# Kernel tuning notes

Measured on AMD Instinct MI355X. Metric: run time of the kernel, lower is better.

The kernel has to match this reference:

```python
import jax, jax.numpy as jnp
import numpy as np

N, B, F_IN, T = 500, 8, 8, 12      # nodes, batch, in_feats, time_interval
H1 = H2 = H3 = 16                   # GCN layer widths (must be equal; see source bug)
HID = 8                             # per-node GRU hidden
E = 8000                            # edges
HG = N * HID                        # GRU hidden size  = 4000
IG = N * H3                         # GRU input size   = 8000


def setup_inputs() -> dict:
    key = jax.random.key(0)
    ks = jax.random.split(key, 12)
    inputs = jax.random.normal(ks[0], (N, B, F_IN, T), jnp.float32)
    src = jax.random.randint(ks[1], (E,), 0, N)
    dst = jax.random.randint(ks[2], (E,), 0, N)

    def lin(k, fi, fo):
        return jax.random.normal(k, (fi, fo), jnp.float32) / np.float32(np.sqrt(fi))

    W1 = lin(ks[3], F_IN, H1); b1 = jax.random.normal(ks[4], (H1,), jnp.float32) * 0.01
    W2 = lin(ks[5], H1, H2);   b2 = jax.random.normal(ks[6], (H2,), jnp.float32) * 0.01
    W3 = lin(ks[7], H2, H3);   b3 = jax.random.normal(ks[8], (H3,), jnp.float32) * 0.01
    W_ih = jax.random.normal(ks[9], (3 * HG, IG), jnp.float32) / np.float32(np.sqrt(IG))
    W_hh = jax.random.normal(ks[10], (3 * HG, HG), jnp.float32) / np.float32(np.sqrt(HG))
    b_ih = jax.random.normal(ks[11], (3 * HG,), jnp.float32) * 0.01
    b_hh = jnp.zeros((3 * HG,), jnp.float32)
    return {"inputs": inputs, "src": src, "dst": dst,
            "W1": W1, "b1": b1, "W2": W2, "b2": b2, "W3": W3, "b3": b3,
            "W_ih": W_ih, "W_hh": W_hh, "b_ih": b_ih, "b_hh": b_hh}


def reference(inputs, src, dst, W1, b1, W2, b2, W3, b3, W_ih, W_hh, b_ih, b_hh):
    ones_e = jnp.ones((E,), jnp.float32)
    # DGL GraphConv norm='both': D_out^{-1/2} on source, D_in^{-1/2} on dest, degs clamped >= 1
    n_out = jnp.clip(jax.ops.segment_sum(ones_e, src, num_segments=N), 1.0) ** -0.5
    n_in = jnp.clip(jax.ops.segment_sum(ones_e, dst, num_segments=N), 1.0) ** -0.5

    def gconv(x, W, b):  # x: [N, B, F]
        m = x * n_out[:, None, None]
        agg = jax.ops.segment_sum(m[src], dst, num_segments=N)
        return (agg * n_in[:, None, None]) @ W + b

    def gcn(x):  # one timestep [N, B, F_IN] -> [N, B, H3]
        h = jax.nn.relu(gconv(x, W1, b1))
        h = jax.nn.relu(gconv(h, W2, b2))
        return gconv(h, W3, b3)

    g = jax.vmap(gcn)(jnp.moveaxis(inputs, 3, 0))        # [T, N, B, H3]
    x_seq = jnp.transpose(g, (0, 2, 1, 3)).reshape(T, B, IG)  # [T, B, N*H3]

    def step(h, x):  # PyTorch GRU cell, gate order r, z, n
        gi = x @ W_ih.T + b_ih
        gh = h @ W_hh.T + b_hh
        i_r, i_z, i_n = jnp.split(gi, 3, axis=-1)
        h_r, h_z, h_n = jnp.split(gh, 3, axis=-1)
        r = jax.nn.sigmoid(i_r + h_r)
        z = jax.nn.sigmoid(i_z + h_z)
        n = jnp.tanh(i_n + r * h_n)
        return (1.0 - z) * n + z * h, None

    h0 = jnp.zeros((B, HG), inputs.dtype)
    hT, _ = jax.lax.scan(step, h0, x_seq)
    return hT.reshape(B, N, HID)
```

## Files before the change

### kernel.cpp

```cpp
#include <hip/hip_runtime.h>

#define NN 500
#define BB 8
#define FIN 8
#define TT 12
#define HH 16
#define EE 8000
#define HG 4000
#define IG 8000
#define G3 12000
#define MM 96

typedef __attribute__((ext_vector_type(8))) _Float16 half8;
typedef __attribute__((ext_vector_type(4))) _Float16 half4v;
typedef __attribute__((ext_vector_type(4))) float f32x4;

__global__ __launch_bounds__(512) void k_prep(const int* __restrict__ src,
                                              const int* __restrict__ dst,
                                              float* __restrict__ n_out,
                                              float* __restrict__ n_in,
                                              int* __restrict__ row_ptr,
                                              int* __restrict__ edge_src) {
  __shared__ int s_dout[NN];
  __shared__ int s_din[NN];
  __shared__ int s_off[NN + 1];
  int tid = threadIdx.x;
  for (int i = tid; i < NN; i += 512) { s_dout[i] = 0; s_din[i] = 0; }
  __syncthreads();
  for (int e = tid; e < EE; e += 512) {
    atomicAdd(&s_dout[src[e]], 1);
    atomicAdd(&s_din[dst[e]], 1);
  }
  __syncthreads();
  if (tid == 0) {
    int acc = 0;
    for (int n = 0; n < NN; ++n) { s_off[n] = acc; acc += s_din[n]; }
    s_off[NN] = acc;
  }
  __syncthreads();
  for (int i = tid; i < NN; i += 512) {
    int dv = s_dout[i]; if (dv < 1) dv = 1;
    int iv = s_din[i];  if (iv < 1) iv = 1;
    n_out[i] = rsqrtf((float)dv);
    n_in[i]  = rsqrtf((float)iv);
    row_ptr[i] = s_off[i];
  }
  if (tid == 0) row_ptr[NN] = s_off[NN];
  __syncthreads();
  for (int e = tid; e < EE; e += 512) {
    int d = dst[e];
    int pos = atomicAdd(&s_off[d], 1);
    edge_src[pos] = src[e];
  }
}

__global__ __launch_bounds__(256) void k_transpose(const float* __restrict__ in,
                                                   float* __restrict__ out) {
  int idx = blockIdx.x * 256 + threadIdx.x;
  if (idx >= TT * NN * BB * FIN) return;
  int f = idx % FIN;
  int b = (idx / FIN) % BB;
  int n = (idx / (FIN * BB)) % NN;
  int t = idx / (FIN * BB * NN);
  out[idx] = in[((n * BB + b) * FIN + f) * TT + t];
}

template <int FI, int FO, bool RELU, typename OT, bool OUT_SEQ>
__global__ __launch_bounds__(128) void k_gcn(const float* __restrict__ x,
                                             const float* __restrict__ W,
                                             const float* __restrict__ bias,
                                             const float* __restrict__ n_out,
                                             const float* __restrict__ n_in,
                                             const int* __restrict__ row_ptr,
                                             const int* __restrict__ edge_src,
                                             OT* __restrict__ y) {
  int bid = blockIdx.x;
  int t = bid / NN, n = bid % NN;
  __shared__ float sW[FI * FO];
  __shared__ float sB[FO];
  __shared__ float sAgg[BB * FI];
  int tid = threadIdx.x;
  for (int i = tid; i < FI * FO; i += 128) sW[i] = W[i];
  if (tid < FO) sB[tid] = bias[tid];
  int r0 = row_ptr[n], r1 = row_ptr[n + 1];
  if (tid < BB * FI) {
    int b = tid / FI, fi = tid % FI;
    float acc = 0.f;
    for (int p = r0; p < r1; ++p) {
      int s = edge_src[p];
      acc += x[((t * NN + s) * BB + b) * FI + fi] * n_out[s];
    }
    sAgg[tid] = acc * n_in[n];
  }
  __syncthreads();
  if (tid < BB * FO) {
    int b = tid / FO, fo = tid % FO;
    float v = sB[fo];
#pragma unroll
    for (int fi = 0; fi < FI; ++fi) v += sAgg[b * FI + fi] * sW[fi * FO + fo];
    if (RELU) v = fmaxf(v, 0.f);
    int oidx = OUT_SEQ ? (((t * BB + b) * NN + n) * FO + fo)
                       : (((t * NN + n) * BB + b) * FO + fo);
    y[oidx] = (OT)v;
  }
}

__global__ __launch_bounds__(256) void k_cvt_whh(const float* __restrict__ w,
                                                 _Float16* __restrict__ wh) {
  size_t i8 = ((size_t)blockIdx.x * 256 + threadIdx.x) * 8;
  if (i8 >= (size_t)G3 * HG) return;
  float4 a = *(const float4*)(w + i8);
  float4 b = *(const float4*)(w + i8 + 4);
  half8 h;
  h[0] = (_Float16)a.x; h[1] = (_Float16)a.y; h[2] = (_Float16)a.z; h[3] = (_Float16)a.w;
  h[4] = (_Float16)b.x; h[5] = (_Float16)b.y; h[6] = (_Float16)b.z; h[7] = (_Float16)b.w;
  *(half8*)(wh + i8) = h;
}

__global__ __launch_bounds__(256, 3) void k_gemm_gi_mfma(const _Float16* __restrict__ Xh,
                                                         const float* __restrict__ Wih,
                                                         float* __restrict__ gip) {
  __shared__ _Float16 sXh[96 * 40];
  __shared__ _Float16 sWh[32 * 40];
  int tid = threadIdx.x;
  int wave = tid >> 6, lane = tid & 63;
  int jb = blockIdx.x * 32;
  int kbase = blockIdx.y * 4000;

  int xrow[3], xc4[3];
  const ushort4* px[3];
#pragma unroll
  for (int i = 0; i < 3; ++i) {
    int idx = i * 256 + tid;
    xrow[i] = idx >> 3; xc4[i] = idx & 7;
    px[i] = (const ushort4*)(Xh + (size_t)xrow[i] * IG + kbase + xc4[i] * 4);
  }
  int wrow = tid >> 3, wc4 = tid & 7;
  const float4* pw = (const float4*)(Wih + (size_t)(jb + wrow) * IG + kbase + wc4 * 4);

  int jt = wave & 1;
  int mh = wave >> 1;
  f32x4 acc[3] = {{0.f,0.f,0.f,0.f},{0.f,0.f,0.f,0.f},{0.f,0.f,0.f,0.f}};

  ushort4 xr[3]; float4 wr;
#pragma unroll
  for (int i = 0; i < 3; ++i) xr[i] = px[i][0];
  wr = pw[0];

  int l15 = lane & 15;
  int colh = (lane >> 4) * 8;

  for (int c = 0; c < 125; ++c) {
    __syncthreads();
#pragma unroll
    for (int i = 0; i < 3; ++i)
      *(ushort4*)&sXh[xrow[i] * 40 + xc4[i] * 4] = xr[i];
    {
      half4v h;
      h[0] = (_Float16)wr.x; h[1] = (_Float16)wr.y;
      h[2] = (_Float16)wr.z; h[3] = (_Float16)wr.w;
      *(half4v*)&sWh[wrow * 40 + wc4 * 4] = h;
    }
    __syncthreads();
    if (c < 124) {
#pragma unroll
      for (int i = 0; i < 3; ++i) xr[i] = px[i][(c + 1) * 8];
      wr = pw[(c + 1) * 8];
    }
    half8 bfrag = *(const half8*)&sWh[(jt * 16 + l15) * 40 + colh];
#pragma unroll
    for (int t = 0; t < 3; ++t) {
      half8 afrag = *(const half8*)&sXh[(mh * 48 + t * 16 + l15) * 40 + colh];
      acc[t] = __builtin_amdgcn_mfma_f32_16x16x32_f16(afrag, bfrag, acc[t], 0, 0, 0);
    }
  }

  float* out = gip + (size_t)blockIdx.y * (MM * G3);
  int j = jb + jt * 16 + l15;
#pragma unroll
  for (int t = 0; t < 3; ++t) {
    int mb = mh * 48 + t * 16 + (lane >> 4) * 4;
#pragma unroll
    for (int r = 0; r < 4; ++r)
      out[(size_t)(mb + r) * G3 + j] = acc[t][r];
  }
}

__device__ __forceinline__ int swz2(int f) { return f ^ (((f >> 4) & 7) << 1); }

__global__ __launch_bounds__(256) void k_gemm_gh(const float* __restrict__ ht,
                                                 const _Float16* __restrict__ Whh_h,
                                                 float* __restrict__ ghp) {
  int j0 = blockIdx.x * 96;
  int ks = blockIdx.y;
  int kbase = ks * 1000;
  __shared__ float4 sH4[2000];
  int tid = threadIdx.x;
  const float4* H4 = (const float4*)ht;
#pragma unroll
  for (int l = 0; l < 8; ++l) {
    int f = l * 256 + tid;
    if (f < 2000) sH4[swz2(f)] = H4[kbase * 2 + f];
  }
  __syncthreads();
  int jl = tid >> 3;
  int k8 = tid & 7;
  const half8* W0 = (const half8*)(Whh_h + (size_t)(j0 + jl)      * HG + kbase);
  const half8* W1 = (const half8*)(Whh_h + (size_t)(j0 + jl + 32) * HG + kbase);
  const half8* W2 = (const half8*)(Whh_h + (size_t)(j0 + jl + 64) * HG + kbase);
  float acc[3][8] = {};
  for (int i = 0; i < 16; ++i) {
    int kq = i * 8 + k8;
    if (kq < 125) {
      half8 w0 = W0[kq], w1 = W1[kq], w2 = W2[kq];
#pragma unroll
      for (int kk = 0; kk < 8; ++kk) {
        int f = (kq * 8 + kk) * 2;
        float4 ha = sH4[swz2(f)];
        float4 hb = sH4[swz2(f + 1)];
        float hm[8] = {ha.x, ha.y, ha.z, ha.w, hb.x, hb.y, hb.z, hb.w};
        float v0 = (float)w0[kk], v1 = (float)w1[kk], v2 = (float)w2[kk];
#pragma unroll
        for (int m = 0; m < 8; ++m) {
          acc[0][m] += hm[m] * v0;
          acc[1][m] += hm[m] * v1;
          acc[2][m] += hm[m] * v2;
        }
      }
    }
  }
#pragma unroll
  for (int r = 0; r < 3; ++r)
#pragma unroll
    for (int m = 0; m < 8; ++m) {
      float v = acc[r][m];
      v += __shfl_down(v, 4, 8);
      v += __shfl_down(v, 2, 8);
      v += __shfl_down(v, 1, 8);
      acc[r][m] = v;
    }
  if (k8 == 0) {
    float* outp = ghp + (size_t)ks * (BB * G3);
#pragma unroll
    for (int r = 0; r < 3; ++r) {
      int j = j0 + jl + r * 32;
#pragma unroll
      for (int m = 0; m < 8; ++m) outp[m * G3 + j] = acc[r][m];
    }
  }
}

__global__ __launch_bounds__(256) void k_gates0(const float* __restrict__ gip,
                                                const float* __restrict__ b_ih,
                                                const float* __restrict__ b_hh,
                                                float* __restrict__ h32n) {
  int idx = blockIdx.x * 256 + threadIdx.x;
  int q = idx >> 3, m = idx & 7;
  const float* g0 = gip + (size_t)m * G3;
  const float* g1 = gip + (size_t)MM * G3 + (size_t)m * G3;
  float ir  = b_ih[q]          + g0[q]          + g1[q];
  float iz  = b_ih[q + HG]     + g0[q + HG]     + g1[q + HG];
  float in_ = b_ih[q + 2*HG]   + g0[q + 2*HG]   + g1[q + 2*HG];
  float r = 1.f / (1.f + __expf(-(ir + b_hh[q])));
  float z = 1.f / (1.f + __expf(-(iz + b_hh[q + HG])));
  float nn = tanhf(in_ + r * b_hh[q + 2*HG]);
  h32n[idx] = (1.f - z) * nn;
}

__global__ __launch_bounds__(256) void k_gates(const float* __restrict__ gip,
                                               const float* __restrict__ ghp,
                                               const float* __restrict__ b_ih,
                                               const float* __restrict__ b_hh,
                                               const float* __restrict__ ht_old,
                                               float* __restrict__ ht_new,
                                               float* __restrict__ hout, int t) {
  int idx = blockIdx.x * 256 + threadIdx.x;
  if (idx >= BB * HG) return;
  int b = idx / HG, q = idx % HG;
  int m = t * BB + b;
  const float* g0 = gip;
  const float* g1 = gip + (size_t)MM * G3;
  float ir = b_ih[q]          + g0[m * G3 + q]          + g1[m * G3 + q];
  float iz = b_ih[q + HG]     + g0[m * G3 + q + HG]     + g1[m * G3 + q + HG];
  float in_ = b_ih[q + 2*HG]  + g0[m * G3 + q + 2*HG]   + g1[m * G3 + q + 2*HG];
  float hr = b_hh[q], hz = b_hh[q + HG], hn = b_hh[q + 2*HG];
#pragma unroll
  for (int s = 0; s < 4; ++s) {
    const float* gh = ghp + (size_t)s * (BB * G3) + b * G3;
    hr += gh[q]; hz += gh[q + HG]; hn += gh[q + 2*HG];
  }
  float r = 1.f / (1.f + __expf(-(ir + hr)));
  float z = 1.f / (1.f + __expf(-(iz + hz)));
  float nn = tanhf(in_ + r * hn);
  float ho = ht_old[q * BB + b];
  float h = (1.f - z) * nn + z * ho;
  ht_new[q * BB + b] = h;
  if (hout) hout[b * HG + q] = h;
}

extern "C" void kernel_launch(void* const* d_in, const int* in_sizes, int n_in,
                              void* d_out, int out_size, void* d_ws, size_t ws_size,
                              hipStream_t stream) {
  const float* x_in = (const float*)d_in[0];
  const int*   src  = (const int*)d_in[1];
  const int*   dst  = (const int*)d_in[2];
  const float* W1   = (const float*)d_in[3];
  const float* b1   = (const float*)d_in[4];
  const float* W2   = (const float*)d_in[5];
  const float* b2   = (const float*)d_in[6];
  const float* W3   = (const float*)d_in[7];
  const float* b3   = (const float*)d_in[8];
  const float* Wih  = (const float*)d_in[9];
  const float* Whh  = (const float*)d_in[10];
  const float* bih  = (const float*)d_in[11];
  const float* bhh  = (const float*)d_in[12];
  float* out = (float*)d_out;

  float* W = (float*)d_ws;
  size_t off = 0;
  float* n_out = W + off; off += 512;
  float* n_in_ = W + off; off += 512;
  float* x0    = W + off; off += (size_t)TT * NN * BB * FIN;
  float* xa    = W + off; off += (size_t)TT * NN * BB * HH;
  float* xb    = W + off; off += (size_t)TT * NN * BB * HH;
  _Float16* xseq = (_Float16*)(W + off); off += (size_t)MM * IG / 2;
  float* gip   = W + off; off += (size_t)2 * MM * G3;
  float* ghp   = W + off; off += (size_t)4 * BB * G3;
  float* ht0   = W + off; off += (size_t)HG * BB;
  float* ht1   = W + off; off += (size_t)HG * BB;
  int* row_ptr  = (int*)(W + off); off += 512;
  int* edge_src = (int*)(W + off); off += 8000;
  off = (off + 3) & ~(size_t)3;
  _Float16* whh_h = (_Float16*)(W + off); off += (size_t)G3 * HG / 2;
  (void)ws_size; (void)in_sizes; (void)n_in; (void)out_size;

  k_cvt_whh<<<((size_t)G3 * HG / 8 + 255) / 256, 256, 0, stream>>>(Whh, whh_h);
  k_prep<<<1, 512, 0, stream>>>(src, dst, n_out, n_in_, row_ptr, edge_src);
  k_transpose<<<(TT * NN * BB * FIN + 255) / 256, 256, 0, stream>>>(x_in, x0);
  k_gcn<FIN, HH, true, float, false><<<TT * NN, 128, 0, stream>>>(x0, W1, b1, n_out, n_in_, row_ptr, edge_src, xa);
  k_gcn<HH, HH, true, float, false><<<TT * NN, 128, 0, stream>>>(xa, W2, b2, n_out, n_in_, row_ptr, edge_src, xb);
  k_gcn<HH, HH, false, _Float16, true><<<TT * NN, 128, 0, stream>>>(xb, W3, b3, n_out, n_in_, row_ptr, edge_src, xseq);
  k_gemm_gi_mfma<<<dim3(375, 2), 256, 0, stream>>>(xseq, Wih, gip);

  k_gates0<<<BB * HG / 256, 256, 0, stream>>>(gip, bih, bhh, ht0);

  float* hcur = ht0;
  float* hnxt = ht1;
  for (int t = 1; t < TT; ++t) {
    k_gemm_gh<<<dim3(125, 4), 256, 0, stream>>>(hcur, whh_h, ghp);
    k_gates<<<(BB * HG + 255) / 256, 256, 0, stream>>>(
        gip, ghp, bih, bhh, hcur, hnxt, (t == TT - 1) ? out : nullptr, t);
    float* tmp = hcur; hcur = hnxt; hnxt = tmp;
  }
}
```

Before: 525.9 us.

## Fuse recurrent GEMM and GRU gate update via last-block split-K reduction

Merges the per-timestep hidden-state GEMM and the gate kernel into one kernel. Each block now computes all three gates (r, z, n) for the same 32 hidden units, so the last of the four split-K blocks can reduce the partials and apply the gates in place, using an atomic counter per column group. This removes 11 kernel launches and the separate gate pass's global round trip. In exchange it adds atomics, fences and a counter reset, and the weight row accesses become strided across the three gate blocks.

```diff
diff --git a/kernel.cpp b/kernel.cpp
--- a/kernel.cpp
+++ b/kernel.cpp
@@ -186,70 +186,6 @@
   }
 }
 
-__device__ __forceinline__ int swz2(int f) { return f ^ (((f >> 4) & 7) << 1); }
-
-__global__ __launch_bounds__(256) void k_gemm_gh(const float* __restrict__ ht,
-                                                 const _Float16* __restrict__ Whh_h,
-                                                 float* __restrict__ ghp) {
-  int j0 = blockIdx.x * 96;
-  int ks = blockIdx.y;
-  int kbase = ks * 1000;
-  __shared__ float4 sH4[2000];
-  int tid = threadIdx.x;
-  const float4* H4 = (const float4*)ht;
-#pragma unroll
-  for (int l = 0; l < 8; ++l) {
-    int f = l * 256 + tid;
-    if (f < 2000) sH4[swz2(f)] = H4[kbase * 2 + f];
-  }
-  __syncthreads();
-  int jl = tid >> 3;
-  int k8 = tid & 7;
-  const half8* W0 = (const half8*)(Whh_h + (size_t)(j0 + jl)      * HG + kbase);
-  const half8* W1 = (const half8*)(Whh_h + (size_t)(j0 + jl + 32) * HG + kbase);
-  const half8* W2 = (const half8*)(Whh_h + (size_t)(j0 + jl + 64) * HG + kbase);
-  float acc[3][8] = {};
-  for (int i = 0; i < 16; ++i) {
-    int kq = i * 8 + k8;
-    if (kq < 125) {
-      half8 w0 = W0[kq], w1 = W1[kq], w2 = W2[kq];
-#pragma unroll
-      for (int kk = 0; kk < 8; ++kk) {
-        int f = (kq * 8 + kk) * 2;
-        float4 ha = sH4[swz2(f)];
-        float4 hb = sH4[swz2(f + 1)];
-        float hm[8] = {ha.x, ha.y, ha.z, ha.w, hb.x, hb.y, hb.z, hb.w};
-        float v0 = (float)w0[kk], v1 = (float)w1[kk], v2 = (float)w2[kk];
-#pragma unroll
-        for (int m = 0; m < 8; ++m) {
-          acc[0][m] += hm[m] * v0;
-          acc[1][m] += hm[m] * v1;
-          acc[2][m] += hm[m] * v2;
-        }
-      }
-    }
-  }
-#pragma unroll
-  for (int r = 0; r < 3; ++r)
-#pragma unroll
-    for (int m = 0; m < 8; ++m) {
-      float v = acc[r][m];
-      v += __shfl_down(v, 4, 8);
-      v += __shfl_down(v, 2, 8);
-      v += __shfl_down(v, 1, 8);
-      acc[r][m] = v;
-    }
-  if (k8 == 0) {
-    float* outp = ghp + (size_t)ks * (BB * G3);
-#pragma unroll
-    for (int r = 0; r < 3; ++r) {
-      int j = j0 + jl + r * 32;
-#pragma unroll
-      for (int m = 0; m < 8; ++m) outp[m * G3 + j] = acc[r][m];
-    }
-  }
-}
-
 __global__ __launch_bounds__(256) void k_gates0(const float* __restrict__ gip,
                                                 const float* __restrict__ b_ih,
                                                 const float* __restrict__ b_hh,
@@ -267,35 +203,113 @@
   h32n[idx] = (1.f - z) * nn;
 }
 
-__global__ __launch_bounds__(256) void k_gates(const float* __restrict__ gip,
-                                               const float* __restrict__ ghp,
-                                               const float* __restrict__ b_ih,
-                                               const float* __restrict__ b_hh,
-                                               const float* __restrict__ ht_old,
-                                               float* __restrict__ ht_new,
-                                               float* __restrict__ hout, int t) {
-  int idx = blockIdx.x * 256 + threadIdx.x;
-  if (idx >= BB * HG) return;
-  int b = idx / HG, q = idx % HG;
-  int m = t * BB + b;
-  const float* g0 = gip;
-  const float* g1 = gip + (size_t)MM * G3;
-  float ir = b_ih[q]          + g0[m * G3 + q]          + g1[m * G3 + q];
-  float iz = b_ih[q + HG]     + g0[m * G3 + q + HG]     + g1[m * G3 + q + HG];
-  float in_ = b_ih[q + 2*HG]  + g0[m * G3 + q + 2*HG]   + g1[m * G3 + q + 2*HG];
-  float hr = b_hh[q], hz = b_hh[q + HG], hn = b_hh[q + 2*HG];
-#pragma unroll
-  for (int s = 0; s < 4; ++s) {
-    const float* gh = ghp + (size_t)s * (BB * G3) + b * G3;
-    hr += gh[q]; hz += gh[q + HG]; hn += gh[q + 2*HG];
-  }
-  float r = 1.f / (1.f + __expf(-(ir + hr)));
-  float z = 1.f / (1.f + __expf(-(iz + hz)));
-  float nn = tanhf(in_ + r * hn);
-  float ho = ht_old[q * BB + b];
-  float h = (1.f - z) * nn + z * ho;
-  ht_new[q * BB + b] = h;
-  if (hout) hout[b * HG + q] = h;
+__device__ __forceinline__ int swz2(int f) { return f ^ (((f >> 4) & 7) << 1); }
+
+__global__ __launch_bounds__(256) void k_ghg(const float* __restrict__ ht,
+                                             const _Float16* __restrict__ Whh_h,
+                                             const float* __restrict__ gip,
+                                             const float* __restrict__ b_ih,
+                                             const float* __restrict__ b_hh,
+                                             float* __restrict__ preS,
+                                             int* __restrict__ cnt,
+                                             float* __restrict__ ht_new,
+                                             float* __restrict__ hout, int t) {
+  int qg = blockIdx.x;
+  int ks = blockIdx.y;
+  int kbase = ks * 1000;
+  __shared__ float4 sH4[2000];
+  __shared__ int sLast;
+  int tid = threadIdx.x;
+  const float4* H4 = (const float4*)ht;
+#pragma unroll
+  for (int l = 0; l < 8; ++l) {
+    int f = l * 256 + tid;
+    if (f < 2000) sH4[swz2(f)] = H4[kbase * 2 + f];
+  }
+  __syncthreads();
+  int jl = tid >> 3;
+  int k8 = tid & 7;
+  int q = qg * 32 + jl;
+  const half8* W0 = (const half8*)(Whh_h + (size_t)q            * HG + kbase);
+  const half8* W1 = (const half8*)(Whh_h + (size_t)(q + HG)     * HG + kbase);
+  const half8* W2 = (const half8*)(Whh_h + (size_t)(q + 2 * HG) * HG + kbase);
+  float acc[3][8] = {};
+  for (int i = 0; i < 16; ++i) {
+    int kq = i * 8 + k8;
+    if (kq < 125) {
+      half8 w0 = W0[kq], w1 = W1[kq], w2 = W2[kq];
+#pragma unroll
+      for (int kk = 0; kk < 8; ++kk) {
+        int f = (kq * 8 + kk) * 2;
+        float4 ha = sH4[swz2(f)];
+        float4 hb = sH4[swz2(f + 1)];
+        float hm[8] = {ha.x, ha.y, ha.z, ha.w, hb.x, hb.y, hb.z, hb.w};
+        float v0 = (float)w0[kk], v1 = (float)w1[kk], v2 = (float)w2[kk];
+#pragma unroll
+        for (int m = 0; m < 8; ++m) {
+          acc[0][m] += hm[m] * v0;
+          acc[1][m] += hm[m] * v1;
+          acc[2][m] += hm[m] * v2;
+        }
+      }
+    }
+  }
+#pragma unroll
+  for (int r = 0; r < 3; ++r)
+#pragma unroll
+    for (int m = 0; m < 8; ++m) {
+      float v = acc[r][m];
+      v += __shfl_down(v, 4, 8);
+      v += __shfl_down(v, 2, 8);
+      v += __shfl_down(v, 1, 8);
+      acc[r][m] = v;
+    }
+  if (k8 == 0) {
+    float* slot = preS + (((size_t)ks * HG + q) * 3) * 8;
+#pragma unroll
+    for (int g = 0; g < 3; ++g)
+#pragma unroll
+      for (int m = 0; m < 8; ++m)
+        __hip_atomic_store(&slot[g * 8 + m], acc[g][m],
+                           __ATOMIC_RELAXED, __HIP_MEMORY_SCOPE_AGENT);
+  }
+  __threadfence();
+  __syncthreads();
+  if (tid == 0) {
+    int old = __hip_atomic_fetch_add(&cnt[qg], 1, __ATOMIC_ACQ_REL,
+                                     __HIP_MEMORY_SCOPE_AGENT);
+    sLast = (old == 3) ? 1 : 0;
+  }
+  __syncthreads();
+  if (!sLast) return;
+  __threadfence();
+  {
+    int ql = tid >> 3, m = tid & 7;
+    int qq = qg * 32 + ql;
+    float hr = b_hh[qq], hz = b_hh[qq + HG], hn = b_hh[qq + 2 * HG];
+#pragma unroll
+    for (int s = 0; s < 4; ++s) {
+      const float* sl = preS + (((size_t)s * HG + qq) * 3) * 8;
+      hr += __hip_atomic_load(&sl[0 * 8 + m], __ATOMIC_RELAXED, __HIP_MEMORY_SCOPE_AGENT);
+      hz += __hip_atomic_load(&sl[1 * 8 + m], __ATOMIC_RELAXED, __HIP_MEMORY_SCOPE_AGENT);
+      hn += __hip_atomic_load(&sl[2 * 8 + m], __ATOMIC_RELAXED, __HIP_MEMORY_SCOPE_AGENT);
+    }
+    int mg = t * BB + m;
+    const float* g0 = gip + (size_t)mg * G3;
+    const float* g1 = gip + (size_t)MM * G3 + (size_t)mg * G3;
+    float ir  = b_ih[qq]          + g0[qq]          + g1[qq];
+    float iz  = b_ih[qq + HG]     + g0[qq + HG]     + g1[qq + HG];
+    float in_ = b_ih[qq + 2*HG]   + g0[qq + 2*HG]   + g1[qq + 2*HG];
+    float r = 1.f / (1.f + __expf(-(ir + hr)));
+    float z = 1.f / (1.f + __expf(-(iz + hz)));
+    float nn = tanhf(in_ + r * hn);
+    float ho = ht[qq * BB + m];
+    float h = (1.f - z) * nn + z * ho;
+    ht_new[qq * BB + m] = h;
+    if (hout) hout[m * HG + qq] = h;
+  }
+  if (tid == 0)
+    __hip_atomic_store(&cnt[qg], 0, __ATOMIC_RELAXED, __HIP_MEMORY_SCOPE_AGENT);
 }
 
 extern "C" void kernel_launch(void* const* d_in, const int* in_sizes, int n_in,
@@ -325,15 +339,17 @@
   float* xb    = W + off; off += (size_t)TT * NN * BB * HH;
   _Float16* xseq = (_Float16*)(W + off); off += (size_t)MM * IG / 2;
   float* gip   = W + off; off += (size_t)2 * MM * G3;
-  float* ghp   = W + off; off += (size_t)4 * BB * G3;
+  float* preS  = W + off; off += (size_t)4 * HG * 3 * 8;
   float* ht0   = W + off; off += (size_t)HG * BB;
   float* ht1   = W + off; off += (size_t)HG * BB;
   int* row_ptr  = (int*)(W + off); off += 512;
   int* edge_src = (int*)(W + off); off += 8000;
+  int* cnt      = (int*)(W + off); off += 128;
   off = (off + 3) & ~(size_t)3;
   _Float16* whh_h = (_Float16*)(W + off); off += (size_t)G3 * HG / 2;
   (void)ws_size; (void)in_sizes; (void)n_in; (void)out_size;
 
+  hipMemsetAsync(cnt, 0, 128 * sizeof(int), stream);
   k_cvt_whh<<<((size_t)G3 * HG / 8 + 255) / 256, 256, 0, stream>>>(Whh, whh_h);
   k_prep<<<1, 512, 0, stream>>>(src, dst, n_out, n_in_, row_ptr, edge_src);
   k_transpose<<<(TT * NN * BB * FIN + 255) / 256, 256, 0, stream>>>(x_in, x0);
@@ -347,9 +363,9 @@
   float* hcur = ht0;
   float* hnxt = ht1;
   for (int t = 1; t < TT; ++t) {
-    k_gemm_gh<<<dim3(125, 4), 256, 0, stream>>>(hcur, whh_h, ghp);
-    k_gates<<<(BB * HG + 255) / 256, 256, 0, stream>>>(
-        gip, ghp, bih, bhh, hcur, hnxt, (t == TT - 1) ? out : nullptr, t);
+    k_ghg<<<dim3(125, 4), 256, 0, stream>>>(hcur, whh_h, gip, bih, bhh,
+                                            preS, cnt, hnxt,
+                                            (t == TT - 1) ? out : nullptr, t);
     float* tmp = hcur; hcur = hnxt; hnxt = tmp;
   }
 }
```

New measurement: 1.243 ms. 136% more time.

## Use MFMA for recurrent W_hh GEMM and fuse weight conversion into first step

Applied to the files above, without the earlier changes.

Replaces the scalar-FMA hidden-state GEMM with an MFMA 16x16x32 f16 kernel. The hidden state is now also written as an fp16 [B,HG] copy by the gate kernels to feed it. The separate W_hh fp32->fp16 conversion kernel is removed; the first recurrent step converts and stores the fp16 weights while it computes, saving one full pass over the weights. This cuts ALU work and launches. In exchange the hidden state enters the GEMM in fp16, and half of each MFMA B tile is wasted on padding rows for the batch of 8.

```diff
diff --git a/kernel.cpp b/kernel.cpp
--- a/kernel.cpp
+++ b/kernel.cpp
@@ -105,18 +105,6 @@
   }
 }
 
-__global__ __launch_bounds__(256) void k_cvt_whh(const float* __restrict__ w,
-                                                 _Float16* __restrict__ wh) {
-  size_t i8 = ((size_t)blockIdx.x * 256 + threadIdx.x) * 8;
-  if (i8 >= (size_t)G3 * HG) return;
-  float4 a = *(const float4*)(w + i8);
-  float4 b = *(const float4*)(w + i8 + 4);
-  half8 h;
-  h[0] = (_Float16)a.x; h[1] = (_Float16)a.y; h[2] = (_Float16)a.z; h[3] = (_Float16)a.w;
-  h[4] = (_Float16)b.x; h[5] = (_Float16)b.y; h[6] = (_Float16)b.z; h[7] = (_Float16)b.w;
-  *(half8*)(wh + i8) = h;
-}
-
 __global__ __launch_bounds__(256, 3) void k_gemm_gi_mfma(const _Float16* __restrict__ Xh,
                                                          const float* __restrict__ Wih,
                                                          float* __restrict__ gip) {
@@ -186,74 +174,11 @@
   }
 }
 
-__device__ __forceinline__ int swz2(int f) { return f ^ (((f >> 4) & 7) << 1); }
-
-__global__ __launch_bounds__(256) void k_gemm_gh(const float* __restrict__ ht,
-                                                 const _Float16* __restrict__ Whh_h,
-                                                 float* __restrict__ ghp) {
-  int j0 = blockIdx.x * 96;
-  int ks = blockIdx.y;
-  int kbase = ks * 1000;
-  __shared__ float4 sH4[2000];
-  int tid = threadIdx.x;
-  const float4* H4 = (const float4*)ht;
-#pragma unroll
-  for (int l = 0; l < 8; ++l) {
-    int f = l * 256 + tid;
-    if (f < 2000) sH4[swz2(f)] = H4[kbase * 2 + f];
-  }
-  __syncthreads();
-  int jl = tid >> 3;
-  int k8 = tid & 7;
-  const half8* W0 = (const half8*)(Whh_h + (size_t)(j0 + jl)      * HG + kbase);
-  const half8* W1 = (const half8*)(Whh_h + (size_t)(j0 + jl + 32) * HG + kbase);
-  const half8* W2 = (const half8*)(Whh_h + (size_t)(j0 + jl + 64) * HG + kbase);
-  float acc[3][8] = {};
-  for (int i = 0; i < 16; ++i) {
-    int kq = i * 8 + k8;
-    if (kq < 125) {
-      half8 w0 = W0[kq], w1 = W1[kq], w2 = W2[kq];
-#pragma unroll
-      for (int kk = 0; kk < 8; ++kk) {
-        int f = (kq * 8 + kk) * 2;
-        float4 ha = sH4[swz2(f)];
-        float4 hb = sH4[swz2(f + 1)];
-        float hm[8] = {ha.x, ha.y, ha.z, ha.w, hb.x, hb.y, hb.z, hb.w};
-        float v0 = (float)w0[kk], v1 = (float)w1[kk], v2 = (float)w2[kk];
-#pragma unroll
-        for (int m = 0; m < 8; ++m) {
-          acc[0][m] += hm[m] * v0;
-          acc[1][m] += hm[m] * v1;
-          acc[2][m] += hm[m] * v2;
-        }
-      }
-    }
-  }
-#pragma unroll
-  for (int r = 0; r < 3; ++r)
-#pragma unroll
-    for (int m = 0; m < 8; ++m) {
-      float v = acc[r][m];
-      v += __shfl_down(v, 4, 8);
-      v += __shfl_down(v, 2, 8);
-      v += __shfl_down(v, 1, 8);
-      acc[r][m] = v;
-    }
-  if (k8 == 0) {
-    float* outp = ghp + (size_t)ks * (BB * G3);
-#pragma unroll
-    for (int r = 0; r < 3; ++r) {
-      int j = j0 + jl + r * 32;
-#pragma unroll
-      for (int m = 0; m < 8; ++m) outp[m * G3 + j] = acc[r][m];
-    }
-  }
-}
-
 __global__ __launch_bounds__(256) void k_gates0(const float* __restrict__ gip,
                                                 const float* __restrict__ b_ih,
                                                 const float* __restrict__ b_hh,
-                                                float* __restrict__ h32n) {
+                                                float* __restrict__ h32n,
+                                                _Float16* __restrict__ h_t) {
   int idx = blockIdx.x * 256 + threadIdx.x;
   int q = idx >> 3, m = idx & 7;
   const float* g0 = gip + (size_t)m * G3;
@@ -264,7 +189,75 @@
   float r = 1.f / (1.f + __expf(-(ir + b_hh[q])));
   float z = 1.f / (1.f + __expf(-(iz + b_hh[q + HG])));
   float nn = tanhf(in_ + r * b_hh[q + 2*HG]);
-  h32n[idx] = (1.f - z) * nn;
+  float h = (1.f - z) * nn;
+  h32n[idx] = h;
+  h_t[(size_t)m * HG + q] = (_Float16)h;
+}
+
+__global__ __launch_bounds__(256) void k_ghm(const _Float16* __restrict__ wh,
+                                             const _Float16* __restrict__ h_t,
+                                             float* __restrict__ ghp) {
+  int tid = threadIdx.x;
+  int wave = tid >> 6, lane = tid & 63;
+  int ks = blockIdx.y;
+  int kbase = ks * 1024;
+  int kn = (ks == 3) ? 29 : 32;
+  int l15 = lane & 15;
+  int ko = (lane >> 4) * 8;
+  int row = blockIdx.x * 64 + wave * 16 + l15;
+  int rowc = row < G3 ? row : G3 - 1;
+  const half8* __restrict__ A  = (const half8*)(wh + (size_t)rowc * HG + kbase + ko);
+  const half8* __restrict__ Bp = (const half8*)(h_t + (size_t)(l15 & 7) * HG + kbase + ko);
+  f32x4 acc = {0.f, 0.f, 0.f, 0.f};
+#pragma unroll 4
+  for (int i = 0; i < kn; ++i)
+    acc = __builtin_amdgcn_mfma_f32_16x16x32_f16(A[i * 4], Bp[i * 4], acc, 0, 0, 0);
+  if (l15 < 8) {
+    float* outp = ghp + (size_t)ks * (BB * G3) + (size_t)l15 * G3;
+    int jb = blockIdx.x * 64 + wave * 16 + (lane >> 4) * 4;
+#pragma unroll
+    for (int r = 0; r < 4; ++r) {
+      int j = jb + r;
+      if (j < G3) outp[j] = acc[r];
+    }
+  }
+}
+
+__global__ __launch_bounds__(256) void k_ghcvtm(const float* __restrict__ Whh,
+                                                _Float16* __restrict__ whh_h,
+                                                const _Float16* __restrict__ h_t,
+                                                float* __restrict__ ghp) {
+  int tid = threadIdx.x;
+  int wave = tid >> 6, lane = tid & 63;
+  int ks = blockIdx.y;
+  int kbase = ks * 1024;
+  int kn = (ks == 3) ? 29 : 32;
+  int l15 = lane & 15;
+  int ko = (lane >> 4) * 8;
+  int row = blockIdx.x * 64 + wave * 16 + l15;
+  int rowc = row < G3 ? row : G3 - 1;
+  const float4* __restrict__ F = (const float4*)(Whh + (size_t)rowc * HG + kbase + ko);
+  half8* __restrict__ O = (half8*)(whh_h + (size_t)rowc * HG + kbase + ko);
+  const half8* __restrict__ Bp = (const half8*)(h_t + (size_t)(l15 & 7) * HG + kbase + ko);
+  f32x4 acc = {0.f, 0.f, 0.f, 0.f};
+#pragma unroll 2
+  for (int i = 0; i < kn; ++i) {
+    float4 x = F[i * 8], y = F[i * 8 + 1];
+    half8 a;
+    a[0] = (_Float16)x.x; a[1] = (_Float16)x.y; a[2] = (_Float16)x.z; a[3] = (_Float16)x.w;
+    a[4] = (_Float16)y.x; a[5] = (_Float16)y.y; a[6] = (_Float16)y.z; a[7] = (_Float16)y.w;
+    O[i * 4] = a;
+    acc = __builtin_amdgcn_mfma_f32_16x16x32_f16(a, Bp[i * 4], acc, 0, 0, 0);
+  }
+  if (l15 < 8) {
+    float* outp = ghp + (size_t)ks * (BB * G3) + (size_t)l15 * G3;
+    int jb = blockIdx.x * 64 + wave * 16 + (lane >> 4) * 4;
+#pragma unroll
+    for (int r = 0; r < 4; ++r) {
+      int j = jb + r;
+      if (j < G3) outp[j] = acc[r];
+    }
+  }
 }
 
 __global__ __launch_bounds__(256) void k_gates(const float* __restrict__ gip,
@@ -273,6 +266,7 @@
                                                const float* __restrict__ b_hh,
                                                const float* __restrict__ ht_old,
                                                float* __restrict__ ht_new,
+                                               _Float16* __restrict__ h_t,
                                                float* __restrict__ hout, int t) {
   int idx = blockIdx.x * 256 + threadIdx.x;
   if (idx >= BB * HG) return;
@@ -295,6 +289,7 @@
   float ho = ht_old[q * BB + b];
   float h = (1.f - z) * nn + z * ho;
   ht_new[q * BB + b] = h;
+  h_t[(size_t)b * HG + q] = (_Float16)h;
   if (hout) hout[b * HG + q] = h;
 }
 
@@ -328,13 +323,13 @@
   float* ghp   = W + off; off += (size_t)4 * BB * G3;
   float* ht0   = W + off; off += (size_t)HG * BB;
   float* ht1   = W + off; off += (size_t)HG * BB;
+  _Float16* h_t = (_Float16*)(W + off); off += (size_t)HG * BB / 2;
   int* row_ptr  = (int*)(W + off); off += 512;
   int* edge_src = (int*)(W + off); off += 8000;
   off = (off + 3) & ~(size_t)3;
-  _Float16* whh_h = (_Float16*)(W + off); off += (size_t)G3 * HG / 2;
+  _Float16* whh_h = (_Float16*)(W + off); off += (size_t)G3 * HG / 2 + 64;
   (void)ws_size; (void)in_sizes; (void)n_in; (void)out_size;
 
-  k_cvt_whh<<<((size_t)G3 * HG / 8 + 255) / 256, 256, 0, stream>>>(Whh, whh_h);
   k_prep<<<1, 512, 0, stream>>>(src, dst, n_out, n_in_, row_ptr, edge_src);
   k_transpose<<<(TT * NN * BB * FIN + 255) / 256, 256, 0, stream>>>(x_in, x0);
   k_gcn<FIN, HH, true, float, false><<<TT * NN, 128, 0, stream>>>(x0, W1, b1, n_out, n_in_, row_ptr, edge_src, xa);
@@ -342,14 +337,19 @@
   k_gcn<HH, HH, false, _Float16, true><<<TT * NN, 128, 0, stream>>>(xb, W3, b3, n_out, n_in_, row_ptr, edge_src, xseq);
   k_gemm_gi_mfma<<<dim3(375, 2), 256, 0, stream>>>(xseq, Wih, gip);
 
-  k_gates0<<<BB * HG / 256, 256, 0, stream>>>(gip, bih, bhh, ht0);
+  k_gates0<<<BB * HG / 256, 256, 0, stream>>>(gip, bih, bhh, ht0, h_t);
 
   float* hcur = ht0;
   float* hnxt = ht1;
-  for (int t = 1; t < TT; ++t) {
-    k_gemm_gh<<<dim3(125, 4), 256, 0, stream>>>(hcur, whh_h, ghp);
+  k_ghcvtm<<<dim3(188, 4), 256, 0, stream>>>(Whh, whh_h, h_t, ghp);
+  k_gates<<<(BB * HG + 255) / 256, 256, 0, stream>>>(
+      gip, ghp, bih, bhh, hcur, hnxt, h_t, nullptr, 1);
+  { float* tmp = hcur; hcur = hnxt; hnxt = tmp; }
+
+  for (int t = 2; t < TT; ++t) {
+    k_ghm<<<dim3(188, 4), 256, 0, stream>>>(whh_h, h_t, ghp);
     k_gates<<<(BB * HG + 255) / 256, 256, 0, stream>>>(
-        gip, ghp, bih, bhh, hcur, hnxt, (t == TT - 1) ? out : nullptr, t);
+        gip, ghp, bih, bhh, hcur, hnxt, h_t, (t == TT - 1) ? out : nullptr, t);
     float* tmp = hcur; hcur = hnxt; hnxt = tmp;
   }
 }
```

After: 471.1 us. -10.4%, faster.
